# Kernel tuning notes

Hardware: AMD Instinct MI355X
Metric: run time of the kernel (lower is better)

The kernel has to match this reference:

```python
import jax, jax.numpy as jnp
import numpy as np

D_MODEL = 1024
D_FF = 4096
NUM_EXPERTS = 8
TOP_K = 2  # expert_capacity


def setup_inputs() -> dict:
    key = jax.random.key(0)
    ks = jax.random.split(key, 7)
    s_in = 1.0 / np.sqrt(D_MODEL)
    s_ff = 1.0 / np.sqrt(D_FF)
    x = jax.random.normal(ks[0], (2, 2048, D_MODEL), dtype=jnp.float32)
    gate_w = jax.random.uniform(ks[1], (NUM_EXPERTS, D_MODEL), jnp.float32, -s_in, s_in)
    gate_b = jax.random.uniform(ks[2], (NUM_EXPERTS,), jnp.float32, -s_in, s_in)
    w1 = jax.random.uniform(ks[3], (NUM_EXPERTS, D_MODEL, D_FF), jnp.float32, -s_in, s_in)
    b1 = jax.random.uniform(ks[4], (NUM_EXPERTS, D_FF), jnp.float32, -s_in, s_in)
    w2 = jax.random.uniform(ks[5], (NUM_EXPERTS, D_FF, D_MODEL), jnp.float32, -s_ff, s_ff)
    b2 = jax.random.uniform(ks[6], (NUM_EXPERTS, D_MODEL), jnp.float32, -s_ff, s_ff)
    return {"x": x, "gate_w": gate_w, "gate_b": gate_b,
            "w1": w1, "b1": b1, "w2": w2, "b2": b2}


def reference(x, gate_w, gate_b, w1, b1, w2, b2):
    E = gate_w.shape[0]
    # Router
    logits = jnp.einsum('bsd,ed->bse', x, gate_w) + gate_b  # [B,S,E]
    top_vals, top_idx = jax.lax.top_k(logits, TOP_K)        # [B,S,K]
    top_w = jax.nn.softmax(top_vals, axis=-1)               # softmax over the top-k logits
    probs = jax.nn.softmax(logits, axis=-1)
    usage = probs.mean(axis=(0, 1))                         # [E]
    load_balancing_loss = E * jnp.sum(usage ** 2) - 1.0
    # Combine weights: sum over top-k slots of weight * one_hot(expert)
    combine = jnp.sum(top_w[..., None] * jax.nn.one_hot(top_idx, E, dtype=x.dtype), axis=2)  # [B,S,E]
    # All experts over all tokens (faithful to the naive dense-then-mask module)
    h = jax.nn.gelu(jnp.einsum('bsd,edf->ebsf', x, w1) + b1[:, None, None, :], approximate=False)
    expert_out = jnp.einsum('ebsf,efd->ebsd', h, w2) + b2[:, None, None, :]  # [E,B,S,D]
    output = jnp.einsum('bse,ebsd->bsd', combine, expert_out)
    return output, load_balancing_loss
```

## Files before the change

kernel.cpp:

```cpp
#include <hip/hip_runtime.h>
#include <hip/hip_bf16.h>
#include <math.h>


#define D_MODEL 1024
#define D_FF    4096
#define NE      8
#define NTOK    4096
#define CAP     4096

typedef __attribute__((ext_vector_type(4))) float f32x4;
typedef __attribute__((ext_vector_type(4))) short s16x4;
typedef __attribute__((ext_vector_type(8))) short s16x8;

__device__ __forceinline__ short f2bf(float f) {
    union { float f; unsigned u; } v; v.f = f;
    unsigned r = v.u + 0x7FFFu + ((v.u >> 16) & 1u);
    return (short)(r >> 16);
}

__device__ __forceinline__ float gelu_f(float x) {
    float u = x * x;
    float v = __builtin_fmaf(0.044715f, u, 1.0f);
    float y2 = 1.5957691216057308f * x * v;
    float r = __builtin_amdgcn_rcpf(__expf(y2) + 1.0f);
    return x - x * r;
}

__device__ __forceinline__ void gload16(const void* g, void* l) {
    __builtin_amdgcn_global_load_lds(
        (const __attribute__((address_space(1))) unsigned*)g,
        (__attribute__((address_space(3))) unsigned*)l, 16, 0, 0);
}


struct RouterSmem { float gw[NE][D_MODEL]; float us[NE]; };

__device__ void router_body(
    const float* __restrict__ x, const float* __restrict__ gw,
    const float* __restrict__ gb, float* __restrict__ usage,
    int* __restrict__ eidx, float* __restrict__ wgt, short* __restrict__ xb,
    RouterSmem* sm, int rb, int nblk)
{
    int tid = threadIdx.x;
    for (int i = tid * 4; i < NE * D_MODEL; i += 256 * 4)
        *(f32x4*)&sm->gw[0][i] = *(const f32x4*)(gw + i);
    if (tid < NE) sm->us[tid] = 0.f;
    __syncthreads();

    int wid = tid >> 6, lane = tid & 63;
    int wave_stride = nblk * 4;
    float l_usage[NE];
#pragma unroll
    for (int e = 0; e < NE; e++) l_usage[e] = 0.f;

    for (int t = rb * 4 + wid; t < NTOK; t += wave_stride) {
        const float* xr = x + (size_t)t * D_MODEL;
        short* xbr = xb + (size_t)t * D_MODEL;
        float acc[NE];
#pragma unroll
        for (int e = 0; e < NE; e++) acc[e] = 0.f;
        for (int i = lane * 4; i < D_MODEL; i += 64 * 4) {
            f32x4 xv = *(const f32x4*)(xr + i);
            s16x4 bv;
#pragma unroll
            for (int j = 0; j < 4; j++) bv[j] = f2bf(xv[j]);
            *(s16x4*)(xbr + i) = bv;
#pragma unroll
            for (int e = 0; e < NE; e++) {
                f32x4 gv = *(const f32x4*)&sm->gw[e][i];
                acc[e] += xv[0]*gv[0] + xv[1]*gv[1] + xv[2]*gv[2] + xv[3]*gv[3];
            }
        }
#pragma unroll
        for (int e = 0; e < NE; e++) {
            float a = acc[e];
            for (int off = 32; off; off >>= 1) a += __shfl_down(a, off);
            acc[e] = a;
        }
        if (lane == 0) {
            float logits[NE];
            float mx = -1e30f;
#pragma unroll
            for (int e = 0; e < NE; e++) { logits[e] = acc[e] + gb[e]; mx = fmaxf(mx, logits[e]); }
            float se = 0.f;
            float pe[NE];
#pragma unroll
            for (int e = 0; e < NE; e++) { pe[e] = expf(logits[e] - mx); se += pe[e]; }
            float inv = 1.f / se;
#pragma unroll
            for (int e = 0; e < NE; e++) l_usage[e] += pe[e] * inv;
            int i0 = 0;
#pragma unroll
            for (int e = 1; e < NE; e++) if (logits[e] > logits[i0]) i0 = e;
            int i1 = -1;
#pragma unroll
            for (int e = 0; e < NE; e++) {
                if (e == i0) continue;
                if (i1 < 0 || logits[e] > logits[i1]) i1 = e;
            }
            float w0 = 1.f / (1.f + expf(logits[i1] - logits[i0]));
            eidx[t] = i0 | (i1 << 8);
            wgt[t] = w0;
        }
    }
    if (lane == 0) {
#pragma unroll
        for (int e = 0; e < NE; e++) atomicAdd(&sm->us[e], l_usage[e]);
    }
    __syncthreads();
    if (tid < NE) atomicAdd(&usage[tid], sm->us[tid]);
}

__device__ void transpose_body(
    const float* __restrict__ src, short* __restrict__ dst, int R, int C,
    int bx, int by, int e, float (*tile)[65])
{
    src += (size_t)e * R * C;
    dst += (size_t)e * R * C;
    int c0 = bx * 64, r0 = by * 64;
    int tid = threadIdx.x;
    int lr = tid >> 2, lc = (tid & 3) * 16;

    const float* s = src + (size_t)(r0 + lr) * C + c0 + lc;
#pragma unroll
    for (int j = 0; j < 4; j++)
        *(f32x4*)&tile[lr][lc + j * 4] = *(const f32x4*)(s + j * 4);
    __syncthreads();

    short* d = dst + (size_t)(c0 + lr) * R + r0 + lc;
    s16x8 v0, v1;
#pragma unroll
    for (int j = 0; j < 8; j++) v0[j] = f2bf(tile[lc + j][lr]);
#pragma unroll
    for (int j = 0; j < 8; j++) v1[j] = f2bf(tile[lc + 8 + j][lr]);
    *(s16x8*)d = v0;
    *(s16x8*)(d + 8) = v1;
}

__global__ __launch_bounds__(256) void prep_kernel(
    const float* __restrict__ x, const float* __restrict__ gw,
    const float* __restrict__ gb, float* __restrict__ usage,
    int* __restrict__ eidx, float* __restrict__ wgt, short* __restrict__ xb,
    const float* __restrict__ w1, short* __restrict__ w1t,
    const float* __restrict__ w2, short* __restrict__ w2t)
{
    __shared__ union { RouterSmem r; float tile[64][65]; } sm;
    int b = blockIdx.x;
    if (b < 256) {
        router_body(x, gw, gb, usage, eidx, wgt, xb, &sm.r, b, 256);
    } else if (b < 256 + 8192) {
        int q = b - 256;
        transpose_body(w1, w1t, D_MODEL, D_FF, q & 63, (q >> 6) & 15, q >> 10, sm.tile);
    } else {
        int q = b - 256 - 8192;
        transpose_body(w2, w2t, D_FF, D_MODEL, q & 15, (q >> 4) & 63, q >> 10, sm.tile);
    }
}

__global__ __launch_bounds__(256) void router_kernel(
    const float* __restrict__ x, const float* __restrict__ gw,
    const float* __restrict__ gb, float* __restrict__ usage,
    int* __restrict__ eidx, float* __restrict__ wgt, short* __restrict__ xb)
{
    __shared__ RouterSmem sm;
    router_body(x, gw, gb, usage, eidx, wgt, xb, &sm, blockIdx.x, gridDim.x);
}

__global__ __launch_bounds__(256) void transpose_cvt(
    const float* __restrict__ src, short* __restrict__ dst, int R, int C)
{
    __shared__ float tile[64][65];
    transpose_body(src, dst, R, C, blockIdx.x, blockIdx.y, blockIdx.z, tile);
}

__global__ __launch_bounds__(256) void build_lists(
    const int* __restrict__ eidx, const float* __restrict__ wgt,
    int* __restrict__ cnt, int* __restrict__ tok_list, float* __restrict__ wt_list,
    int* __restrict__ tok2slot, float* __restrict__ wgt_p,
    int* __restrict__ done, int* __restrict__ offsets,
    const float* __restrict__ usage, float* __restrict__ out_loss)
{
    int e = blockIdx.x;
    __shared__ int s_cnt;
    if (threadIdx.x == 0) s_cnt = 0;
    __syncthreads();
    for (int t = threadIdx.x; t < NTOK; t += 256) {
        int p = eidx[t];
        float w0 = wgt[t];
        if (e == 0) wgt_p[t] = w0;
        if ((p & 255) == e) {
            int s = atomicAdd(&s_cnt, 1);
            tok_list[e * CAP + s] = t; wt_list[e * CAP + s] = w0;
            tok2slot[2 * t] = (e << 16) | s;
        }
        if ((p >> 8) == e) {
            int s = atomicAdd(&s_cnt, 1);
            tok_list[e * CAP + s] = t; wt_list[e * CAP + s] = 1.f - w0;
            tok2slot[2 * t + 1] = (e << 16) | s;
        }
    }
    __syncthreads();
    if (threadIdx.x == 0) {
        cnt[e] = s_cnt;
        __threadfence();
        if (atomicAdd(done, 1) == NE - 1) {
            __threadfence();
            int o = 0;
            for (int k = 0; k < NE; k++) { offsets[k] = o; o += cnt[k]; }
            if (out_loss) {
                float s = 0.f;
                for (int k = 0; k < NE; k++) { float u = usage[k] / (float)NTOK; s += u * u; }
                *out_loss = (float)NE * s - 1.f;
            }
        }
    }
}

__global__ void write_loss(const float* __restrict__ usage, float* __restrict__ out_loss)
{
    float s = 0.f;
    for (int e = 0; e < NE; e++) { float u = usage[e] / (float)NTOK; s += u * u; }
    *out_loss = (float)NE * s - 1.f;
}

#define GEMM_STAGE(AS, BS, KT)                       \
    gload16(asrc0 + (KT), &AS[wid * 16][0]);         \
    gload16(asrc1 + (KT), &AS[64 + wid * 16][0]);    \
    gload16(bsrc0 + (KT), &BS[wid * 16][0]);         \
    gload16(bsrc1 + (KT), &BS[64 + wid * 16][0]);

#define GEMM_COMPUTE(AS, BS)                                                   \
    {                                                                          \
        s16x8 a[4], b[4];                                                      \
        int cidx = (kgr ^ ((lrow >> 1) & 3)) * 8;                              \
        _Pragma("unroll")                                                      \
        for (int i = 0; i < 4; i++) {                                          \
            a[i] = *(const s16x8*)&AS[wr * 64 + i * 16 + lrow][cidx];          \
            b[i] = *(const s16x8*)&BS[wc * 64 + i * 16 + lrow][cidx];          \
        }                                                                      \
        _Pragma("unroll")                                                      \
        for (int i = 0; i < 4; i++)                                            \
            _Pragma("unroll")                                                  \
            for (int j = 0; j < 4; j++)                                        \
                acc[i][j] = __builtin_amdgcn_mfma_f32_16x16x32_bf16(           \
                    a[i], b[j], acc[i][j], 0, 0, 0);                           \
    }

__global__ __launch_bounds__(256) void gemm1_kernel(
    const short* __restrict__ XB, const short* __restrict__ W1T,
    const float* __restrict__ b1, const int* __restrict__ cnt,
    const int* __restrict__ offsets, const int* __restrict__ tok_list,
    short* __restrict__ H)
{
    int r = blockIdx.x;
    int s = (r & 7) * 1024 + (r >> 3);
    int bx = s & 31;
    int by = s >> 5;
    int e  = by >> 5;
    int tm = by & 31;
    int ce = cnt[e];
    if (tm * 128 >= ce) return;
    int n0 = bx * 128;

    __shared__ __align__(16) short As[128][32];
    __shared__ __align__(16) short Bs[128][32];

    int tid = threadIdx.x;
    int lane = tid & 63, wid = tid >> 6;
    int wr = wid >> 1, wc = wid & 1;
    int lrow = lane & 15, kgr = lane >> 4;

    int srow = wid * 16 + (lane >> 2);
    int scol = ((lane & 3) ^ ((lane >> 3) & 3)) * 8;
    int am0 = tm * 128 + srow, am1 = am0 + 64;
    int tok0 = tok_list[e * CAP + (am0 < ce ? am0 : 0)];
    int tok1 = tok_list[e * CAP + (am1 < ce ? am1 : 0)];
    const short* asrc0 = XB + (size_t)tok0 * D_MODEL + scol;
    const short* asrc1 = XB + (size_t)tok1 * D_MODEL + scol;
    const short* bsrc0 = W1T + ((size_t)e * D_FF + n0 + srow) * D_MODEL + scol;
    const short* bsrc1 = bsrc0 + (size_t)64 * D_MODEL;

    f32x4 acc[4][4] = {};
    for (int kt = 0; kt < D_MODEL; kt += 32) {
        GEMM_STAGE(As, Bs, kt);
        __syncthreads();
        GEMM_COMPUTE(As, Bs);
        __syncthreads();
    }

    int offe = offsets[e];
    float bn[4];
#pragma unroll
    for (int j = 0; j < 4; j++) bn[j] = b1[e * D_FF + n0 + wc * 64 + j * 16 + lrow];
#pragma unroll
    for (int i = 0; i < 4; i++) {
#pragma unroll
        for (int q = 0; q < 4; q++) {
            int m = tm * 128 + wr * 64 + i * 16 + kgr * 4 + q;
            if (m >= ce) continue;
            short* hrow = H + (size_t)(offe + m) * D_FF;
#pragma unroll
            for (int j = 0; j < 4; j++) {
                int n = n0 + wc * 64 + j * 16 + lrow;
                hrow[n] = f2bf(gelu_f(acc[i][j][q] + bn[j]));
            }
        }
    }
}

__global__ __launch_bounds__(256) void gemm2_y_kernel(
    const short* __restrict__ H, const short* __restrict__ W2T,
    const float* __restrict__ b2, const int* __restrict__ cnt,
    const int* __restrict__ offsets, float* __restrict__ Y)
{
    int r = blockIdx.x;
    int s = (r & 7) * 256 + (r >> 3);
    int bx = s & 7;
    int by = s >> 3;
    int e  = by >> 5;
    int tm = by & 31;
    int ce = cnt[e];
    if (tm * 128 >= ce) return;
    int offe = offsets[e];
    int n0 = bx * 128;

    __shared__ __align__(16) short As[128][32];
    __shared__ __align__(16) short Bs[128][32];

    int tid = threadIdx.x;
    int lane = tid & 63, wid = tid >> 6;
    int wr = wid >> 1, wc = wid & 1;
    int lrow = lane & 15, kgr = lane >> 4;

    int srow = wid * 16 + (lane >> 2);
    int scol = ((lane & 3) ^ ((lane >> 3) & 3)) * 8;
    int am0 = tm * 128 + srow, am1 = am0 + 64;
    const short* asrc0 = H + (size_t)(offe + (am0 < ce ? am0 : 0)) * D_FF + scol;
    const short* asrc1 = H + (size_t)(offe + (am1 < ce ? am1 : 0)) * D_FF + scol;
    const short* bsrc0 = W2T + ((size_t)e * D_MODEL + n0 + srow) * D_FF + scol;
    const short* bsrc1 = bsrc0 + (size_t)64 * D_FF;

    f32x4 acc[4][4] = {};
    for (int kt = 0; kt < D_FF; kt += 32) {
        GEMM_STAGE(As, Bs, kt);
        __syncthreads();
        GEMM_COMPUTE(As, Bs);
        __syncthreads();
    }

    float bn[4];
#pragma unroll
    for (int j = 0; j < 4; j++) bn[j] = b2[e * D_MODEL + n0 + wc * 64 + j * 16 + lrow];
#pragma unroll
    for (int i = 0; i < 4; i++) {
#pragma unroll
        for (int q = 0; q < 4; q++) {
            int m = tm * 128 + wr * 64 + i * 16 + kgr * 4 + q;
            if (m >= ce) continue;
            float* yrow = Y + (size_t)(offe + m) * D_MODEL;
#pragma unroll
            for (int j = 0; j < 4; j++) {
                int n = n0 + wc * 64 + j * 16 + lrow;
                yrow[n] = acc[i][j][q] + bn[j];
            }
        }
    }
}

__global__ __launch_bounds__(256) void combine_kernel(
    const float* __restrict__ Y, const int* __restrict__ tok2slot,
    const float* __restrict__ wgt_p, const int* __restrict__ offsets,
    float* __restrict__ out)
{
    int t = blockIdx.x;
    int d = threadIdx.x * 4;
    int p0 = tok2slot[2 * t], p1 = tok2slot[2 * t + 1];
    int s0 = offsets[p0 >> 16] + (p0 & 0xFFFF);
    int s1 = offsets[p1 >> 16] + (p1 & 0xFFFF);
    float w0 = wgt_p[t], w1 = 1.f - w0;
    f32x4 a = *(const f32x4*)(Y + (size_t)s0 * D_MODEL + d);
    f32x4 b = *(const f32x4*)(Y + (size_t)s1 * D_MODEL + d);
    f32x4 r;
#pragma unroll
    for (int j = 0; j < 4; j++) r[j] = w0 * a[j] + w1 * b[j];
    *(f32x4*)(out + (size_t)t * D_MODEL + d) = r;
}

__global__ __launch_bounds__(256) void gemm2_kernel(
    const short* __restrict__ H, const short* __restrict__ W2T,
    const float* __restrict__ b2, const int* __restrict__ cnt,
    const int* __restrict__ offsets, const int* __restrict__ tok_list,
    const float* __restrict__ wt_list, float* __restrict__ out)
{
    int e  = blockIdx.y >> 5;
    int tm = blockIdx.y & 31;
    int ce = cnt[e];
    if (tm * 128 >= ce) return;
    int offe = offsets[e];
    int n0 = blockIdx.x * 128;
    int kz = blockIdx.z;
    const int KSPAN = D_FF / 2;
    int kbase = kz * KSPAN;

    __shared__ __align__(16) short As[128][32];
    __shared__ __align__(16) short Bs[128][32];

    int tid = threadIdx.x;
    int lane = tid & 63, wid = tid >> 6;
    int wr = wid >> 1, wc = wid & 1;
    int lrow = lane & 15, kgr = lane >> 4;

    int srow = wid * 16 + (lane >> 2);
    int scol = ((lane & 3) ^ ((lane >> 3) & 3)) * 8;
    int am0 = tm * 128 + srow, am1 = am0 + 64;
    const short* asrc0 = H + (size_t)(offe + (am0 < ce ? am0 : 0)) * D_FF + kbase + scol;
    const short* asrc1 = H + (size_t)(offe + (am1 < ce ? am1 : 0)) * D_FF + kbase + scol;
    const short* bsrc0 = W2T + ((size_t)e * D_MODEL + n0 + srow) * D_FF + kbase + scol;
    const short* bsrc1 = bsrc0 + (size_t)64 * D_FF;

    f32x4 acc[4][4] = {};
    for (int kt = 0; kt < KSPAN; kt += 32) {
        GEMM_STAGE(As, Bs, kt);
        __syncthreads();
        GEMM_COMPUTE(As, Bs);
        __syncthreads();
    }

    float bn[4];
#pragma unroll
    for (int j = 0; j < 4; j++)
        bn[j] = (kz == 0) ? b2[e * D_MODEL + n0 + wc * 64 + j * 16 + lrow] : 0.f;
#pragma unroll
    for (int i = 0; i < 4; i++) {
#pragma unroll
        for (int q = 0; q < 4; q++) {
            int m = tm * 128 + wr * 64 + i * 16 + kgr * 4 + q;
            if (m >= ce) continue;
            int tokm = tok_list[e * CAP + m];
            float wt = wt_list[e * CAP + m];
            float* orow = out + (size_t)tokm * D_MODEL;
#pragma unroll
            for (int j = 0; j < 4; j++) {
                int n = n0 + wc * 64 + j * 16 + lrow;
                atomicAdd(&orow[n], wt * (acc[i][j][q] + bn[j]));
            }
        }
    }
}

extern "C" void kernel_launch(void* const* d_in, const int* in_sizes, int n_in,
                              void* d_out, int out_size, void* d_ws, size_t ws_size,
                              hipStream_t stream)
{
    const float* x  = (const float*)d_in[0];
    const float* gw = (const float*)d_in[1];
    const float* gb = (const float*)d_in[2];
    const float* w1 = (const float*)d_in[3];
    const float* b1 = (const float*)d_in[4];
    const float* w2 = (const float*)d_in[5];
    const float* b2 = (const float*)d_in[6];
    float* out = (float*)d_out;

    char* w = (char*)d_ws;
    int*   cnt      = (int*)(w + 0);
    float* usage    = (float*)(w + 32);
    int*   offsets  = (int*)(w + 64);
    int*   done     = (int*)(w + 96);
    int*   tok_list = (int*)(w + 128);
    float* wt_list  = (float*)(w + 128 + 131072);
    int*   tok2slot = (int*)(w + 128 + 262144);
    float* wgt_p    = (float*)(w + 128 + 262144 + 32768);
    const size_t MB64 = 67108864ull;
    short* XB       = (short*)d_out;
    float* out_loss = out + (size_t)NTOK * D_MODEL;

    size_t need_sep = 311424 + 3ull * MB64;
    size_t need_y1  = 311424 + 2ull * MB64 + 33554432ull;
    hipMemsetAsync(d_ws, 0, 128, stream);

    if (ws_size >= need_sep) {
        short* W1T = (short*)(w + 311424);
        short* W2T = (short*)(w + 311424 + MB64);
        short* H   = (short*)(w + 311424 + 2 * MB64);
        float* Y   = (float*)W1T;
        int*   eidx = (int*)H;
        float* wgt  = (float*)((char*)H + 16384);

        prep_kernel<<<256 + 8192 + 8192, 256, 0, stream>>>(
            x, gw, gb, usage, eidx, wgt, XB, w1, W1T, w2, W2T);
        build_lists<<<NE, 256, 0, stream>>>(
            eidx, wgt, cnt, tok_list, wt_list, tok2slot, wgt_p,
            done, offsets, usage, out_loss);
        gemm1_kernel<<<(D_FF / 128) * NE * (CAP / 128), 256, 0, stream>>>(
            XB, W1T, b1, cnt, offsets, tok_list, H);
        gemm2_y_kernel<<<2048, 256, 0, stream>>>(H, W2T, b2, cnt, offsets, Y);
        combine_kernel<<<NTOK, 256, 0, stream>>>(Y, tok2slot, wgt_p, offsets, out);
        return;
    }

    short* WT  = (short*)(w + 311424);
    short* H   = (short*)(w + 311424 + MB64);
    float* Y   = (float*)(w + 311424 + 2 * MB64);
    bool   use_y = ws_size >= need_y1;
    int*   eidx = (int*)WT;
    float* wgt  = (float*)(WT + NTOK * 2);

    router_kernel<<<256, 256, 0, stream>>>(x, gw, gb, usage, eidx, wgt, XB);
    build_lists<<<NE, 256, 0, stream>>>(
        eidx, wgt, cnt, tok_list, wt_list, tok2slot, wgt_p,
        done, offsets, usage, nullptr);

    transpose_cvt<<<dim3(D_FF / 64, D_MODEL / 64, NE), 256, 0, stream>>>(w1, WT, D_MODEL, D_FF);
    gemm1_kernel<<<(D_FF / 128) * NE * (CAP / 128), 256, 0, stream>>>(
        XB, WT, b1, cnt, offsets, tok_list, H);
    transpose_cvt<<<dim3(D_MODEL / 64, D_FF / 64, NE), 256, 0, stream>>>(w2, WT, D_FF, D_MODEL);

    if (use_y) {
        write_loss<<<1, 1, 0, stream>>>(usage, out_loss);
        gemm2_y_kernel<<<2048, 256, 0, stream>>>(H, WT, b2, cnt, offsets, Y);
        combine_kernel<<<NTOK, 256, 0, stream>>>(Y, tok2slot, wgt_p, offsets, out);
    } else {
        hipMemsetAsync(d_out, 0, (size_t)out_size * sizeof(float), stream);
        write_loss<<<1, 1, 0, stream>>>(usage, out_loss);
        gemm2_kernel<<<dim3(D_MODEL / 128, NE * (CAP / 128), 2), 256, 0, stream>>>(
            H, WT, b2, cnt, offsets, tok_list, wt_list, out);
    }
}
```

Baseline: 316.0 us.

## Move w2 transpose from prep kernel into gemm1 launch to overlap with GEMM

The w2 fp32-to-bf16 transpose blocks move out of the prep kernel and are appended as extra blocks of the gemm1 launch, sharing LDS through a union. The memory-bound transpose can then run alongside the compute-bound first GEMM instead of before it. gemm1 blocks for empty token tiles exit early, which frees slots for the transpose blocks. The trade-off is larger LDS per block (the union is sized for the bigger member) and the two workloads competing for bandwidth.

```diff
diff --git a/kernel.cpp b/kernel.cpp
--- a/kernel.cpp
+++ b/kernel.cpp
@@ -142,19 +142,15 @@
     const float* __restrict__ x, const float* __restrict__ gw,
     const float* __restrict__ gb, float* __restrict__ usage,
     int* __restrict__ eidx, float* __restrict__ wgt, short* __restrict__ xb,
-    const float* __restrict__ w1, short* __restrict__ w1t,
-    const float* __restrict__ w2, short* __restrict__ w2t)
+    const float* __restrict__ w1, short* __restrict__ w1t)
 {
     __shared__ union { RouterSmem r; float tile[64][65]; } sm;
     int b = blockIdx.x;
     if (b < 256) {
         router_body(x, gw, gb, usage, eidx, wgt, xb, &sm.r, b, 256);
-    } else if (b < 256 + 8192) {
+    } else {
         int q = b - 256;
         transpose_body(w1, w1t, D_MODEL, D_FF, q & 63, (q >> 6) & 15, q >> 10, sm.tile);
-    } else {
-        int q = b - 256 - 8192;
-        transpose_body(w2, w2t, D_FF, D_MODEL, q & 15, (q >> 4) & 63, q >> 10, sm.tile);
     }
 }
 
@@ -251,6 +247,80 @@
     const short* __restrict__ XB, const short* __restrict__ W1T,
     const float* __restrict__ b1, const int* __restrict__ cnt,
     const int* __restrict__ offsets, const int* __restrict__ tok_list,
+    short* __restrict__ H,
+    const float* __restrict__ w2, short* __restrict__ w2t)
+{
+    __shared__ union {
+        struct { __align__(16) short As[128][32]; __align__(16) short Bs[128][32]; } g;
+        float tile[64][65];
+    } sm;
+
+    if (blockIdx.x >= 8192) {
+        int q = blockIdx.x - 8192;
+        transpose_body(w2, w2t, D_FF, D_MODEL, q & 15, (q >> 4) & 63, q >> 10, sm.tile);
+        return;
+    }
+
+    int r = blockIdx.x;
+    int s = (r & 7) * 1024 + (r >> 3);
+    int bx = s & 31;
+    int by = s >> 5;
+    int e  = by >> 5;
+    int tm = by & 31;
+    int ce = cnt[e];
+    if (tm * 128 >= ce) return;
+    int n0 = bx * 128;
+
+    short (&As)[128][32] = sm.g.As;
+    short (&Bs)[128][32] = sm.g.Bs;
+
+    int tid = threadIdx.x;
+    int lane = tid & 63, wid = tid >> 6;
+    int wr = wid >> 1, wc = wid & 1;
+    int lrow = lane & 15, kgr = lane >> 4;
+
+    int srow = wid * 16 + (lane >> 2);
+    int scol = ((lane & 3) ^ ((lane >> 3) & 3)) * 8;
+    int am0 = tm * 128 + srow, am1 = am0 + 64;
+    int tok0 = tok_list[e * CAP + (am0 < ce ? am0 : 0)];
+    int tok1 = tok_list[e * CAP + (am1 < ce ? am1 : 0)];
+    const short* asrc0 = XB + (size_t)tok0 * D_MODEL + scol;
+    const short* asrc1 = XB + (size_t)tok1 * D_MODEL + scol;
+    const short* bsrc0 = W1T + ((size_t)e * D_FF + n0 + srow) * D_MODEL + scol;
+    const short* bsrc1 = bsrc0 + (size_t)64 * D_MODEL;
+
+    f32x4 acc[4][4] = {};
+    for (int kt = 0; kt < D_MODEL; kt += 32) {
+        GEMM_STAGE(As, Bs, kt);
+        __syncthreads();
+        GEMM_COMPUTE(As, Bs);
+        __syncthreads();
+    }
+
+    int offe = offsets[e];
+    float bn[4];
+#pragma unroll
+    for (int j = 0; j < 4; j++) bn[j] = b1[e * D_FF + n0 + wc * 64 + j * 16 + lrow];
+#pragma unroll
+    for (int i = 0; i < 4; i++) {
+#pragma unroll
+        for (int q = 0; q < 4; q++) {
+            int m = tm * 128 + wr * 64 + i * 16 + kgr * 4 + q;
+            if (m >= ce) continue;
+            short* hrow = H + (size_t)(offe + m) * D_FF;
+#pragma unroll
+            for (int j = 0; j < 4; j++) {
+                int n = n0 + wc * 64 + j * 16 + lrow;
+                hrow[n] = f2bf(gelu_f(acc[i][j][q] + bn[j]));
+            }
+        }
+    }
+}
+
+__global__ __launch_bounds__(256) void gemm1_plain(
+    const short* __restrict__ XB, const short* __restrict__ W1T,
+    const float* __restrict__ b1, const int* __restrict__ cnt,
+    const int* __restrict__ offsets, const int* __restrict__ tok_list,
     short* __restrict__ H)
 {
     int r = blockIdx.x;
@@ -487,13 +557,13 @@
         int*   eidx = (int*)H;
         float* wgt  = (float*)((char*)H + 16384);
 
-        prep_kernel<<<256 + 8192 + 8192, 256, 0, stream>>>(
-            x, gw, gb, usage, eidx, wgt, XB, w1, W1T, w2, W2T);
+        prep_kernel<<<256 + 8192, 256, 0, stream>>>(
+            x, gw, gb, usage, eidx, wgt, XB, w1, W1T);
         build_lists<<<NE, 256, 0, stream>>>(
             eidx, wgt, cnt, tok_list, wt_list, tok2slot, wgt_p,
             done, offsets, usage, out_loss);
-        gemm1_kernel<<<(D_FF / 128) * NE * (CAP / 128), 256, 0, stream>>>(
-            XB, W1T, b1, cnt, offsets, tok_list, H);
+        gemm1_kernel<<<8192 + 8192, 256, 0, stream>>>(
+            XB, W1T, b1, cnt, offsets, tok_list, H, w2, W2T);
         gemm2_y_kernel<<<2048, 256, 0, stream>>>(H, W2T, b2, cnt, offsets, Y);
         combine_kernel<<<NTOK, 256, 0, stream>>>(Y, tok2slot, wgt_p, offsets, out);
         return;
@@ -512,8 +582,7 @@
         done, offsets, usage, nullptr);
 
     transpose_cvt<<<dim3(D_FF / 64, D_MODEL / 64, NE), 256, 0, stream>>>(w1, WT, D_MODEL, D_FF);
-    gemm1_kernel<<<(D_FF / 128) * NE * (CAP / 128), 256, 0, stream>>>(
-        XB, WT, b1, cnt, offsets, tok_list, H);
+    gemm1_plain<<<8192, 256, 0, stream>>>(XB, WT, b1, cnt, offsets, tok_list, H);
     transpose_cvt<<<dim3(D_MODEL / 64, D_FF / 64, NE), 256, 0, stream>>>(w2, WT, D_FF, D_MODEL);
 
     if (use_y) {
```

Measured after the change: 325.3 us. +3.0%, slower.

## Rewrite gemm1 with 256x256 tiles, double-buffered LDS and interleaved prefetch

Applied to the files above, without the earlier changes.

Replaces the expert GEMM1 kernel with a 512-thread, 256x256-tile version using a K-step of 64 and two LDS buffers. Loads for the next K-step are issued in four parts between MFMA phases, with explicit vmcnt waits, raw barriers and s_setprio, so global loads overlap compute. Larger tiles raise data reuse per block but use 128KB of LDS and more accumulator registers, which limits occupancy and wastes more work on partially filled token tiles.

```diff
diff --git a/kernel.cpp b/kernel.cpp
--- a/kernel.cpp
+++ b/kernel.cpp
@@ -32,6 +32,9 @@
         (const __attribute__((address_space(1))) unsigned*)g,
         (__attribute__((address_space(3))) unsigned*)l, 16, 0, 0);
 }
+
+#define FENCE asm volatile("" ::: "memory")
+#define BARRIER do { FENCE; __builtin_amdgcn_s_barrier(); FENCE; } while (0)
 
 
 struct RouterSmem { float gw[NE][D_MODEL]; float us[NE]; };
@@ -222,6 +225,121 @@
     float s = 0.f;
     for (int e = 0; e < NE; e++) { float u = usage[e] / (float)NTOK; s += u * u; }
     *out_loss = (float)NE * s - 1.f;
+}
+
+__global__ __launch_bounds__(512, 2) void gemm1_kernel(
+    const short* __restrict__ XB, const short* __restrict__ W1T,
+    const float* __restrict__ b1, const int* __restrict__ cnt,
+    const int* __restrict__ offsets, const int* __restrict__ tok_list,
+    short* __restrict__ H)
+{
+    int r = blockIdx.x;
+    int s = (r & 7) * 256 + (r >> 3);
+    int bx = s & 15;
+    int by = s >> 4;
+    int e  = by >> 4;
+    int tm = by & 15;
+    int ce = cnt[e];
+    if (tm * 256 >= ce) return;
+    int n0 = bx * 256;
+
+    __shared__ __align__(16) short As[2][256][64];
+    __shared__ __align__(16) short Bs[2][256][64];
+
+    int tid = threadIdx.x;
+    int lane = tid & 63, w64 = tid >> 6;
+    int wr = w64 >> 2, wc = w64 & 3;
+    int lrow = lane & 15, kgr = lane >> 4;
+
+    int gc = (lane & 7) ^ (lane >> 3);
+    const short* apt[4];
+    const short* bpt[4];
+#pragma unroll
+    for (int h = 0; h < 2; h++) {
+#pragma unroll
+        for (int j = 0; j < 2; j++) {
+            int rw = h * 128 + j * 64 + w64 * 8 + (lane >> 3);
+            int am = tm * 256 + rw;
+            int tok = tok_list[e * CAP + (am < ce ? am : 0)];
+            apt[h * 2 + j] = XB + (size_t)tok * D_MODEL + gc * 8;
+            bpt[h * 2 + j] = W1T + ((size_t)e * D_FF + n0 + rw) * D_MODEL + gc * 8;
+        }
+    }
+
+#define ISSUE_A(NB, HH, KT)                                                    \
+    gload16(apt[(HH)*2+0] + (KT), (char*)&As[NB][(HH)*128][0] + w64*1024);     \
+    gload16(apt[(HH)*2+1] + (KT), (char*)&As[NB][(HH)*128][0] + 8192 + w64*1024);
+#define ISSUE_B(NB, HH, KT)                                                    \
+    gload16(bpt[(HH)*2+0] + (KT), (char*)&Bs[NB][(HH)*128][0] + w64*1024);     \
+    gload16(bpt[(HH)*2+1] + (KT), (char*)&Bs[NB][(HH)*128][0] + 8192 + w64*1024);
+
+#define PHASE_MFMA(BUF, S, MH)                                                 \
+    {                                                                          \
+        s16x8 a[4], b[4];                                                      \
+        int cc = (((S) * 4 + kgr) ^ (lrow & 7)) * 8;                           \
+        _Pragma("unroll")                                                      \
+        for (int j2 = 0; j2 < 4; j2++)                                         \
+            b[j2] = *(const s16x8*)&Bs[BUF][wc * 64 + j2 * 16 + lrow][cc];     \
+        _Pragma("unroll")                                                      \
+        for (int i2 = 0; i2 < 4; i2++)                                         \
+            a[i2] = *(const s16x8*)&As[BUF][wr * 128 + ((MH)*4+i2)*16 + lrow][cc]; \
+        __builtin_amdgcn_s_setprio(1);                                         \
+        _Pragma("unroll")                                                      \
+        for (int i2 = 0; i2 < 4; i2++)                                         \
+            _Pragma("unroll")                                                  \
+            for (int j2 = 0; j2 < 4; j2++)                                     \
+                acc[(MH)*4+i2][j2] = __builtin_amdgcn_mfma_f32_16x16x32_bf16(  \
+                    a[i2], b[j2], acc[(MH)*4+i2][j2], 0, 0, 0);                \
+        __builtin_amdgcn_s_setprio(0);                                         \
+    }
+
+    f32x4 acc[8][4] = {};
+
+    ISSUE_A(0, 0, 0); ISSUE_A(0, 1, 0); ISSUE_B(0, 0, 0); ISSUE_B(0, 1, 0);
+
+    const int NT = D_MODEL / 64;
+    for (int T = 0; T < NT; T++) {
+        int buf = T & 1, nb = buf ^ 1;
+        int ktn = (T + 1) * 64;
+        bool more = (T + 1) < NT;
+        if (more) { ISSUE_A(nb, 0, ktn); }
+        if (more) { asm volatile("s_waitcnt vmcnt(2)" ::: "memory"); }
+        else      { asm volatile("s_waitcnt vmcnt(0)" ::: "memory"); }
+        BARRIER;
+        PHASE_MFMA(buf, 0, 0);
+        BARRIER;
+        if (more) { ISSUE_A(nb, 1, ktn); }
+        PHASE_MFMA(buf, 0, 1);
+        BARRIER;
+        if (more) { ISSUE_B(nb, 0, ktn); }
+        PHASE_MFMA(buf, 1, 0);
+        BARRIER;
+        if (more) { ISSUE_B(nb, 1, ktn); }
+        PHASE_MFMA(buf, 1, 1);
+        BARRIER;
+    }
+
+    int offe = offsets[e];
+    float bn[4];
+#pragma unroll
+    for (int j = 0; j < 4; j++) bn[j] = b1[e * D_FF + n0 + wc * 64 + j * 16 + lrow];
+#pragma unroll
+    for (int i = 0; i < 8; i++) {
+#pragma unroll
+        for (int q = 0; q < 4; q++) {
+            int m = tm * 256 + wr * 128 + i * 16 + kgr * 4 + q;
+            if (m >= ce) continue;
+            short* hrow = H + (size_t)(offe + m) * D_FF;
+#pragma unroll
+            for (int j = 0; j < 4; j++) {
+                int n = n0 + wc * 64 + j * 16 + lrow;
+                hrow[n] = f2bf(gelu_f(acc[i][j][q] + bn[j]));
+            }
+        }
+    }
+#undef ISSUE_A
+#undef ISSUE_B
+#undef PHASE_MFMA
 }
 
 #define GEMM_STAGE(AS, BS, KT)                       \
@@ -247,68 +365,6 @@
                     a[i], b[j], acc[i][j], 0, 0, 0);                           \
     }
 
-__global__ __launch_bounds__(256) void gemm1_kernel(
-    const short* __restrict__ XB, const short* __restrict__ W1T,
-    const float* __restrict__ b1, const int* __restrict__ cnt,
-    const int* __restrict__ offsets, const int* __restrict__ tok_list,
-    short* __restrict__ H)
-{
-    int r = blockIdx.x;
-    int s = (r & 7) * 1024 + (r >> 3);
-    int bx = s & 31;
-    int by = s >> 5;
-    int e  = by >> 5;
-    int tm = by & 31;
-    int ce = cnt[e];
-    if (tm * 128 >= ce) return;
-    int n0 = bx * 128;
-
-    __shared__ __align__(16) short As[128][32];
-    __shared__ __align__(16) short Bs[128][32];
-
-    int tid = threadIdx.x;
-    int lane = tid & 63, wid = tid >> 6;
-    int wr = wid >> 1, wc = wid & 1;
-    int lrow = lane & 15, kgr = lane >> 4;
-
-    int srow = wid * 16 + (lane >> 2);
-    int scol = ((lane & 3) ^ ((lane >> 3) & 3)) * 8;
-    int am0 = tm * 128 + srow, am1 = am0 + 64;
-    int tok0 = tok_list[e * CAP + (am0 < ce ? am0 : 0)];
-    int tok1 = tok_list[e * CAP + (am1 < ce ? am1 : 0)];
-    const short* asrc0 = XB + (size_t)tok0 * D_MODEL + scol;
-    const short* asrc1 = XB + (size_t)tok1 * D_MODEL + scol;
-    const short* bsrc0 = W1T + ((size_t)e * D_FF + n0 + srow) * D_MODEL + scol;
-    const short* bsrc1 = bsrc0 + (size_t)64 * D_MODEL;
-
-    f32x4 acc[4][4] = {};
-    for (int kt = 0; kt < D_MODEL; kt += 32) {
-        GEMM_STAGE(As, Bs, kt);
-        __syncthreads();
-        GEMM_COMPUTE(As, Bs);
-        __syncthreads();
-    }
-
-    int offe = offsets[e];
-    float bn[4];
-#pragma unroll
-    for (int j = 0; j < 4; j++) bn[j] = b1[e * D_FF + n0 + wc * 64 + j * 16 + lrow];
-#pragma unroll
-    for (int i = 0; i < 4; i++) {
-#pragma unroll
-        for (int q = 0; q < 4; q++) {
-            int m = tm * 128 + wr * 64 + i * 16 + kgr * 4 + q;
-            if (m >= ce) continue;
-            short* hrow = H + (size_t)(offe + m) * D_FF;
-#pragma unroll
-            for (int j = 0; j < 4; j++) {
-                int n = n0 + wc * 64 + j * 16 + lrow;
-                hrow[n] = f2bf(gelu_f(acc[i][j][q] + bn[j]));
-            }
-        }
-    }
-}
-
 __global__ __launch_bounds__(256) void gemm2_y_kernel(
     const short* __restrict__ H, const short* __restrict__ W2T,
     const float* __restrict__ b2, const int* __restrict__ cnt,
@@ -492,7 +548,7 @@
         build_lists<<<NE, 256, 0, stream>>>(
             eidx, wgt, cnt, tok_list, wt_list, tok2slot, wgt_p,
             done, offsets, usage, out_loss);
-        gemm1_kernel<<<(D_FF / 128) * NE * (CAP / 128), 256, 0, stream>>>(
+        gemm1_kernel<<<2048, 512, 0, stream>>>(
             XB, W1T, b1, cnt, offsets, tok_list, H);
         gemm2_y_kernel<<<2048, 256, 0, stream>>>(H, W2T, b2, cnt, offsets, Y);
         combine_kernel<<<NTOK, 256, 0, stream>>>(Y, tok2slot, wgt_p, offsets, out);
@@ -512,8 +568,7 @@
         done, offsets, usage, nullptr);
 
     transpose_cvt<<<dim3(D_FF / 64, D_MODEL / 64, NE), 256, 0, stream>>>(w1, WT, D_MODEL, D_FF);
-    gemm1_kernel<<<(D_FF / 128) * NE * (CAP / 128), 256, 0, stream>>>(
-        XB, WT, b1, cnt, offsets, tok_list, H);
+    gemm1_kernel<<<2048, 512, 0, stream>>>(XB, WT, b1, cnt, offsets, tok_list, H);
     transpose_cvt<<<dim3(D_MODEL / 64, D_FF / 64, NE), 256, 0, stream>>>(w2, WT, D_FF, D_MODEL);
 
     if (use_y) {
```

Result: slower. 370.0 us (+17.1%).
